# Optimization experiments

Measured on AMD Instinct MI355X. Metric: run time of the kernel, lower is better.

Reference implementation:

```python
import jax, jax.numpy as jnp
from jax import lax
import numpy as np

B, C_IN, F, T = 8, 16, 1024, 512
D = 1024          # rnn_hidden_size == rnn_input_size
L = 4             # rnn_num_layers
N_TOKENS = 512
RES_REDUCE = 2


def setup_inputs() -> dict:
    key = jax.random.key(0)
    ks = jax.random.split(key, 8)
    fused_feats = jax.random.normal(ks[0], (B, C_IN, F, T), dtype=jnp.float32)
    s_audio_length = jax.random.randint(ks[1], (B,), 1, T + 1, dtype=jnp.int64)
    # 1x1 conv: C_IN -> 1 channel
    conv_w = jax.random.normal(ks[2], (C_IN,), dtype=jnp.float32) * (1.0 / np.sqrt(C_IN))
    conv_b = jnp.zeros((1,), dtype=jnp.float32)
    # SRU per-layer params (all layers have d_in == D): W [L, D, 3D], v [L, 2D], b [L, 2D]
    sru_W = jax.random.normal(ks[3], (L, D, 3 * D), dtype=jnp.float32) * (1.0 / np.sqrt(D))
    sru_v = jax.random.normal(ks[4], (L, 2 * D), dtype=jnp.float32) * 0.1
    sru_b = jnp.zeros((L, 2 * D), dtype=jnp.float32)
    fc_w = jax.random.normal(ks[5], (D, N_TOKENS), dtype=jnp.float32) * (1.0 / np.sqrt(D))
    fc_b = jnp.zeros((N_TOKENS,), dtype=jnp.float32)
    return dict(fused_feats=fused_feats, s_audio_length=s_audio_length,
                conv_w=conv_w, conv_b=conv_b,
                sru_W=sru_W, sru_v=sru_v, sru_b=sru_b,
                fc_w=fc_w, fc_b=fc_b)


def _sru_layer(x, W, v, b):
    # x: [T, B, D]; W: [D, 3D]; v, b: [2D]
    d = W.shape[1] // 3
    U = jnp.einsum('tbi,ik->tbk', x, W).reshape(x.shape[0], x.shape[1], 3, d)
    x_tilde, f_pre, r_pre = U[..., 0, :], U[..., 1, :], U[..., 2, :]
    vf, vr = v[:d], v[d:]
    bf, br = b[:d], b[d:]

    def step(c, inp):
        xt_t, fp_t = inp
        f = jax.nn.sigmoid(fp_t + vf * c + bf)
        c_new = f * c + (1.0 - f) * xt_t
        return c_new, c_new

    c0 = jnp.zeros((x.shape[1], d), dtype=x.dtype)
    _, cs = lax.scan(step, c0, (x_tilde, f_pre))            # cs: [T, B, D]
    r = jax.nn.sigmoid(r_pre + vr * cs + br)                # reset uses c_t
    return r * cs + (1.0 - r) * x                           # highway residual


def reference(fused_feats, s_audio_length, conv_w, conv_b, sru_W, sru_v, sru_b, fc_w, fc_b):
    # 1x1 conv over channel dim + ReLU: [B, C, F, T] -> [B, F, T]
    x = jax.nn.relu(jnp.einsum('bcft,c->bft', fused_feats, conv_w) + conv_b[0])
    x = x.transpose(2, 0, 1)                                # [T, B, F]
    for l in range(L):
        x = _sru_layer(x, sru_W[l], sru_v[l], sru_b[l])
    rnn_out = x.transpose(1, 0, 2)                          # [B, T, D]
    tokens_logits = jnp.einsum('btd,dk->btk', rnn_out, fc_w) + fc_b
    return tokens_logits, s_audio_length // RES_REDUCE
```

## Files before the change

kernel.cpp:

```cpp
#include <hip/hip_runtime.h>
#include <cstddef>
#include <cstdint>

static constexpr int B_  = 8;
static constexpr int CIN = 16;
static constexpr int F_  = 1024;
static constexpr int T_  = 512;
static constexpr int D_  = 1024;
static constexpr int L_  = 4;
static constexpr int NT  = 512;
static constexpr int M_  = T_ * B_;
static constexpr int K3  = 3 * D_;
static constexpr int NP  = 4 * D_;

typedef __attribute__((ext_vector_type(8))) short short8;
typedef __attribute__((ext_vector_type(4))) float floatx4;

__device__ __forceinline__ unsigned short f2bf(float f) {
    unsigned int u = __builtin_bit_cast(unsigned int, f);
    u += 0x7FFFu + ((u >> 16) & 1u);
    return (unsigned short)(u >> 16);
}
__device__ __forceinline__ float bf2f(unsigned short s) {
    unsigned int u = ((unsigned int)s) << 16;
    return __builtin_bit_cast(float, u);
}

#define GLD16(g, l)                                                              \
    __builtin_amdgcn_global_load_lds(                                            \
        (__attribute__((address_space(1))) unsigned int*)(g),                    \
        (__attribute__((address_space(3))) unsigned int*)(l), 16, 0, 0)

__global__ __launch_bounds__(256) void conv_relu_tr(
    const float* __restrict__ feats, const float* __restrict__ wv,
    const float* __restrict__ bv, unsigned short* __restrict__ x0) {
    __shared__ float tile[32][68];
    const int b  = blockIdx.z;
    const int f0 = blockIdx.y * 32;
    const int t0 = blockIdx.x * 64;
    const float bias = bv[0];

    const int t4 = threadIdx.x & 15;
    const int fi = threadIdx.x >> 4;
    #pragma unroll
    for (int fo = 0; fo < 32; fo += 16) {
        const int f = fo + fi;
        float4 acc = {bias, bias, bias, bias};
        const float* p = feats + (((size_t)b * CIN) * F_ + (f0 + f)) * T_ + t0 + t4 * 4;
        #pragma unroll
        for (int c = 0; c < CIN; ++c) {
            const float4 vv = *(const float4*)(p + (size_t)c * F_ * T_);
            const float w = wv[c];
            acc.x += w * vv.x; acc.y += w * vv.y;
            acc.z += w * vv.z; acc.w += w * vv.w;
        }
        acc.x = fmaxf(acc.x, 0.f); acc.y = fmaxf(acc.y, 0.f);
        acc.z = fmaxf(acc.z, 0.f); acc.w = fmaxf(acc.w, 0.f);
        *(float4*)&tile[f][t4 * 4] = acc;
    }
    __syncthreads();
    const int f4 = threadIdx.x & 7;
    const int tr = threadIdx.x >> 3;
    #pragma unroll
    for (int to = 0; to < 64; to += 32) {
        const int t = to + tr;
        unsigned short pk[4];
        #pragma unroll
        for (int q = 0; q < 4; ++q) pk[q] = f2bf(tile[f4 * 4 + q][t]);
        *(uint2*)&x0[(size_t)(t0 + t) * (B_ * D_) + (size_t)b * D_ + f0 + f4 * 4] =
            *(const uint2*)pk;
    }
}

__global__ __launch_bounds__(256) void prep_weights(
    const float* __restrict__ sru_W, const float* __restrict__ fc_w,
    unsigned short* __restrict__ Wt, unsigned short* __restrict__ WtF) {
    __shared__ float tile[32][33];
    const int z  = blockIdx.z;
    const int x  = threadIdx.x & 31;
    const int y8 = threadIdx.x >> 5;
    if (z < 16) {
        const int l = z >> 2, j = z & 3;
        const int d0 = blockIdx.x * 32;
        const int k0 = blockIdx.y * 32;
        unsigned short* Wo = Wt + (size_t)l * ((size_t)NP * D_);
        if (j < 3) {
            const float* W = sru_W + (size_t)l * D_ * K3;
            #pragma unroll
            for (int yo = 0; yo < 32; yo += 8)
                tile[yo + y8][x] = W[(size_t)(k0 + yo + y8) * K3 + j * D_ + d0 + x];
            __syncthreads();
            #pragma unroll
            for (int yo = 0; yo < 32; yo += 8) {
                const int dy = yo + y8;
                Wo[(size_t)((d0 + dy) * 4 + j) * D_ + k0 + x] = f2bf(tile[x][dy]);
            }
        } else {
            #pragma unroll
            for (int yo = 0; yo < 32; yo += 8) {
                const int dy = d0 + yo + y8;
                Wo[(size_t)(dy * 4 + 3) * D_ + k0 + x] =
                    (k0 + x == dy) ? (unsigned short)0x3F80u : (unsigned short)0u;
            }
        }
    } else {
        if (blockIdx.x >= NT / 32) return;
        const int n0 = blockIdx.x * 32;
        const int k0 = blockIdx.y * 32;
        #pragma unroll
        for (int yo = 0; yo < 32; yo += 8)
            tile[yo + y8][x] = fc_w[(size_t)(k0 + yo + y8) * NT + n0 + x];
        __syncthreads();
        #pragma unroll
        for (int yo = 0; yo < 32; yo += 8)
            WtF[(size_t)(n0 + yo + y8) * D_ + k0 + x] = f2bf(tile[x][yo + y8]);
    }
}

__global__ __launch_bounds__(256) void gemm_fc(
    const unsigned short* __restrict__ A,
    const unsigned short* __restrict__ Bt,
    float* __restrict__ Cv, const float* __restrict__ bias,
    const int* __restrict__ lens, float* __restrict__ lout,
    int N, int K) {
    __shared__ unsigned short As[128 * 32];
    __shared__ unsigned short Bs[128 * 32];

    const int tid  = threadIdx.x;
    const int lane = tid & 63;
    const int wid  = tid >> 6;
    const int m0 = blockIdx.y * 128;
    const int n0 = blockIdx.x * 128;
    const int wm = (wid >> 1) * 64;
    const int wn = (wid & 1) * 64;

    if (blockIdx.x == 0 && blockIdx.y == 0 && tid < B_)
        lout[tid] = (float)(lens[tid] >> 1);

    floatx4 acc[4][4];
    #pragma unroll
    for (int mi = 0; mi < 4; ++mi)
        #pragma unroll
        for (int ni = 0; ni < 4; ++ni)
            acc[mi][ni] = (floatx4){0.f, 0.f, 0.f, 0.f};

    const char* gA = (const char*)A;
    const char* gB = (const char*)Bt;
    const size_t rowstride = (size_t)K * 2;
    const size_t rA0 = (size_t)(m0 + (tid >> 2)) * rowstride + (tid & 3) * 16;
    const size_t rB0 = (size_t)(n0 + (tid >> 2)) * rowstride + (tid & 3) * 16;
    const size_t pstep = 64 * rowstride;
    char* sA = (char*)As;
    char* sB = (char*)Bs;
    const int ldsbase = wid * 1024;

    const int rsel = lane & 15;
    const int koff = (lane >> 4) * 16;

    for (int k0 = 0; k0 < K; k0 += 32) {
        const size_t kb = (size_t)k0 * 2;
        GLD16(gA + rA0 + kb,         sA + ldsbase);
        GLD16(gA + rA0 + kb + pstep, sA + ldsbase + 4096);
        GLD16(gB + rB0 + kb,         sB + ldsbase);
        GLD16(gB + rB0 + kb + pstep, sB + ldsbase + 4096);
        __syncthreads();

        short8 af[4], bfv[4];
        #pragma unroll
        for (int mi = 0; mi < 4; ++mi)
            af[mi] = *(const short8*)(sA + ((wm + mi * 16 + rsel) * 64 + koff));
        #pragma unroll
        for (int ni = 0; ni < 4; ++ni)
            bfv[ni] = *(const short8*)(sB + ((wn + ni * 16 + rsel) * 64 + koff));
        #pragma unroll
        for (int mi = 0; mi < 4; ++mi)
            #pragma unroll
            for (int ni = 0; ni < 4; ++ni)
                acc[mi][ni] = __builtin_amdgcn_mfma_f32_16x16x32_bf16(
                    af[mi], bfv[ni], acc[mi][ni], 0, 0, 0);
        __syncthreads();
    }

    const int cl = lane & 15;
    const int qr = lane >> 4;
    #pragma unroll
    for (int mi = 0; mi < 4; ++mi) {
        #pragma unroll
        for (int ni = 0; ni < 4; ++ni) {
            const int gn = n0 + wn + ni * 16 + cl;
            #pragma unroll
            for (int i = 0; i < 4; ++i) {
                const int gm = m0 + wm + mi * 16 + qr * 4 + i;
                const int t  = gm >> 3;
                const int bb = gm & 7;
                Cv[((size_t)bb * T_ + t) * NT + gn] = acc[mi][ni][i] + bias[gn];
            }
        }
    }
}

#define KT_BODY(CB, PB, KT2, DO_STAGE)                                        \
    {                                                                         \
        if (DO_STAGE) {      \
            const size_t gk = (size_t)(KT2) * 64;                             \
            _Pragma("unroll") for (int s = 0; s < 2; ++s)                     \
                GLD16(Ab + (size_t)grow[s] * 2048 + gk + gcol[s],             \
                      (PB) + ((s * 8 + wid) << 10));                          \
        }                                                                     \
        short8 af[8], bf01[2], bf23[2];                                       \
        _Pragma("unroll") for (int mi = 0; mi < 8; ++mi)                      \
            af[mi] = *(const short8*)((CB) + aoff[mi]);                       \
        _Pragma("unroll") for (int ni = 0; ni < 2; ++ni)                      \
            bf01[ni] = *(const short8*)((CB) + boff[ni]);                     \
        __builtin_amdgcn_s_setprio(1);                                        \
        _Pragma("unroll") for (int mi = 0; mi < 8; ++mi)                      \
            _Pragma("unroll") for (int ni = 0; ni < 2; ++ni)                  \
                acc[mi][ni] = __builtin_amdgcn_mfma_f32_16x16x32_bf16(        \
                    af[mi], bf01[ni], acc[mi][ni], 0, 0, 0);                  \
        __builtin_amdgcn_s_setprio(0);                                        \
        __builtin_amdgcn_s_barrier();                                         \
        if (DO_STAGE) {      \
            const size_t gk = (size_t)(KT2) * 64;                             \
            _Pragma("unroll") for (int s = 0; s < 2; ++s)                     \
                GLD16(Bb + (size_t)grow[s] * 2048 + gk + gcol[s],             \
                      (PB) + 16384 + ((s * 8 + wid) << 10));                  \
        }                                                                     \
        _Pragma("unroll") for (int ni = 0; ni < 2; ++ni)                      \
            bf23[ni] = *(const short8*)((CB) + boff[2 + ni]);                 \
        __builtin_amdgcn_s_setprio(1);                                        \
        _Pragma("unroll") for (int mi = 0; mi < 8; ++mi)                      \
            _Pragma("unroll") for (int ni = 0; ni < 2; ++ni)                  \
                acc[mi][2 + ni] = __builtin_amdgcn_mfma_f32_16x16x32_bf16(    \
                    af[mi], bf23[ni], acc[mi][2 + ni], 0, 0, 0);              \
        __builtin_amdgcn_s_setprio(0);                                        \
    }

__global__ __launch_bounds__(512, 2) void gemm256_gate(
    const unsigned short* __restrict__ A,
    const unsigned short* __restrict__ Bt,
    unsigned short* __restrict__ C) {
    __shared__ unsigned short lds[49152];
    char* const sb = (char*)lds;

    const int tid  = threadIdx.x;
    const int lane = tid & 63;
    const int wid  = tid >> 6;
    const int wm   = wid >> 2;
    const int wn   = wid & 3;
    const int m0   = blockIdx.y * 256;
    const int n0   = blockIdx.x * 256;

    const char* Ab = (const char*)A  + (size_t)m0 * 2048;
    const char* Bb = (const char*)Bt + (size_t)n0 * 2048;

    int grow[2], gcol[2];
    #pragma unroll
    for (int s = 0; s < 2; ++s) {
        const int q  = ((s * 8 + wid) << 10) + lane * 16;
        const int qs = q ^ (((q >> 7) & 3) << 4);
        grow[s] = qs >> 6;
        gcol[s] = qs & 63;
    }
    const int rl = lane & 15;
    const int kb = (lane >> 4) * 16;
    int aoff[8], boff[4];
    #pragma unroll
    for (int mi = 0; mi < 8; ++mi) {
        const int q = (wm * 128 + mi * 16 + rl) * 64 + kb;
        aoff[mi] = q ^ (((q >> 7) & 3) << 4);
    }
    #pragma unroll
    for (int ni = 0; ni < 4; ++ni) {
        const int q = (wn * 64 + ni * 16 + rl) * 64 + kb;
        boff[ni] = 16384 + (q ^ (((q >> 7) & 3) << 4));
    }

    floatx4 acc[8][4];
    #pragma unroll
    for (int mi = 0; mi < 8; ++mi)
        #pragma unroll
        for (int ni = 0; ni < 4; ++ni)
            acc[mi][ni] = (floatx4){0.f, 0.f, 0.f, 0.f};

    char* const b0 = sb;
    char* const b1 = sb + 32768;
    char* const b2 = sb + 65536;

    #pragma unroll
    for (int t = 0; t < 2; ++t) {
        char* pb = sb + t * 32768;
        const size_t gk = (size_t)t * 64;
        #pragma unroll
        for (int s = 0; s < 2; ++s)
            GLD16(Ab + (size_t)grow[s] * 2048 + gk + gcol[s],
                  pb + ((s * 8 + wid) << 10));
        #pragma unroll
        for (int s = 0; s < 2; ++s)
            GLD16(Bb + (size_t)grow[s] * 2048 + gk + gcol[s],
                  pb + 16384 + ((s * 8 + wid) << 10));
    }
    asm volatile("s_waitcnt vmcnt(4)" ::: "memory");
    __builtin_amdgcn_s_barrier();

    for (int kt = 0; kt < 30; kt += 3) {
        KT_BODY(b0, b2, kt + 2, true);
        asm volatile("s_waitcnt vmcnt(4)" ::: "memory");
        __builtin_amdgcn_s_barrier();
        KT_BODY(b1, b0, kt + 3, true);
        asm volatile("s_waitcnt vmcnt(4)" ::: "memory");
        __builtin_amdgcn_s_barrier();
        KT_BODY(b2, b1, kt + 4, true);
        asm volatile("s_waitcnt vmcnt(4)" ::: "memory");
        __builtin_amdgcn_s_barrier();
    }
    KT_BODY(b0, b2, 0, false);
    asm volatile("s_waitcnt vmcnt(0)" ::: "memory");
    __builtin_amdgcn_s_barrier();
    KT_BODY(b1, b0, 0, false);

    const int cl = lane & 15;
    const int qr = lane >> 4;
    #pragma unroll
    for (int mi = 0; mi < 8; ++mi) {
        #pragma unroll
        for (int ni = 0; ni < 4; ++ni) {
            const int gn = n0 + wn * 64 + ni * 16 + cl;
            #pragma unroll
            for (int i = 0; i < 4; ++i) {
                const int gm = m0 + wm * 128 + mi * 16 + qr * 4 + i;
                C[(size_t)gm * NP + gn] = f2bf(acc[mi][ni][i]);
            }
        }
    }
}

__global__ __launch_bounds__(64) void sru_scan(
    const unsigned short* __restrict__ U4,
    const float* __restrict__ v, const float* __restrict__ bvec,
    unsigned short* __restrict__ h) {
    const int idx = blockIdx.x * 64 + threadIdx.x;
    const int d  = idx & (D_ - 1);

    constexpr float L2E = 1.44269504088896340736f;
    const float vf2  = -v[d] * L2E;
    const float vr2  = -v[D_ + d] * L2E;
    const float mbfL = -bvec[d] * L2E;
    const float mbrL = -bvec[D_ + d] * L2E;

    const uint2* up = (const uint2*)U4 + idx;
    unsigned short* hp = h + idx;

    constexpr int UNR  = 8;
    constexpr int PIPE = 4;
    constexpr int NB   = T_ / UNR;
    constexpr size_t ST = (size_t)B_ * D_;

    uint2 ub[PIPE][UNR];
    #pragma unroll
    for (int p = 0; p < PIPE; ++p)
        #pragma unroll
        for (int j = 0; j < UNR; ++j)
            ub[p][j] = up[(size_t)(p * UNR + j) * ST];

    float c = 0.0f;
    for (int bt = 0; bt < NB; bt += PIPE) {
        #pragma unroll
        for (int p = 0; p < PIPE; ++p) {
            const int s = bt + p;
            #pragma unroll
            for (int j = 0; j < UNR; ++j) {
                const uint2 u = ub[p][j];
                const float xt  = bf2f((unsigned short)(u.x & 0xFFFFu));
                const float fpp = bf2f((unsigned short)(u.x >> 16));
                const float rpp = bf2f((unsigned short)(u.y & 0xFFFFu));
                const float xi  = bf2f((unsigned short)(u.y >> 16));
                const float pre1 = fmaf(fpp, -L2E, mbfL);
                const float pre2 = fmaf(rpp, -L2E, mbrL);
                float e1;
                asm("v_exp_f32 %0, %1" : "=v"(e1) : "v"(fmaf(vf2, c, pre1)));
                const float f  = __builtin_amdgcn_rcpf(1.0f + e1);
                c = fmaf(f, c - xt, xt);
                float e2;
                asm("v_exp_f32 %0, %1" : "=v"(e2) : "v"(fmaf(vr2, c, pre2)));
                const float r  = __builtin_amdgcn_rcpf(1.0f + e2);
                hp[(size_t)(s * UNR + j) * ST] = f2bf(fmaf(r, c - xi, xi));
            }
            if (s + PIPE < NB) {
                #pragma unroll
                for (int j = 0; j < UNR; ++j)
                    ub[p][j] = up[(size_t)((s + PIPE) * UNR + j) * ST];
            }
        }
    }
}

extern "C" void kernel_launch(void* const* d_in, const int* in_sizes, int n_in,
                              void* d_out, int out_size, void* d_ws, size_t ws_size,
                              hipStream_t stream) {
    const float* feats  = (const float*)d_in[0];
    const int*   lens   = (const int*)d_in[1];
    const float* conv_w = (const float*)d_in[2];
    const float* conv_b = (const float*)d_in[3];
    const float* sru_W  = (const float*)d_in[4];
    const float* sru_v  = (const float*)d_in[5];
    const float* sru_b  = (const float*)d_in[6];
    const float* fc_w   = (const float*)d_in[7];
    const float* fc_b   = (const float*)d_in[8];
    float* out = (float*)d_out;

    unsigned short* x0 = (unsigned short*)d_ws;
    unsigned short* x1 = x0 + (size_t)M_ * D_;
    unsigned short* U4 = x1 + (size_t)M_ * D_;
    unsigned short* Wt = U4 + (size_t)M_ * NP;
    unsigned short* WtF = Wt + (size_t)L_ * NP * D_;

    conv_relu_tr<<<dim3(T_ / 64, F_ / 32, B_), 256, 0, stream>>>(
        feats, conv_w, conv_b, x0);

    prep_weights<<<dim3(32, 32, 17), 256, 0, stream>>>(sru_W, fc_w, Wt, WtF);

    unsigned short* cur = x0;
    unsigned short* nxt = x1;
    for (int l = 0; l < L_; ++l) {
        gemm256_gate<<<dim3(NP / 256, M_ / 256), 512, 0, stream>>>(
            cur, Wt + (size_t)l * NP * D_, U4);
        sru_scan<<<(B_ * D_) / 64, 64, 0, stream>>>(
            U4, sru_v + (size_t)l * 2 * D_, sru_b + (size_t)l * 2 * D_, nxt);
        unsigned short* tmp = cur; cur = nxt; nxt = tmp;
    }

    gemm_fc<<<dim3(NT / 128, M_ / 128), 256, 0, stream>>>(
        cur, WtF, out, fc_b, lens, out + (size_t)M_ * NT, NT, D_);
}
```

Before: 709.7 us.

## Drop identity block from gate GEMM and read residual input directly in scan

The gate GEMM used to compute a fourth output block equal to the identity copy of x, so the scan could read all four values packed together. That block is now removed, which cuts the GEMM's N from 4D to 3D with 192-wide tiles, and the scan reads the residual from the layer input buffer instead. The layout becomes interleaved x_tilde/f pairs followed by a separate r block. This saves a quarter of the GEMM FLOPs and the U writes, at the cost of three separate strided loads per step in the scan and a shallower prefetch depth there.

After: 752.6 us. 6.0% more time.

```diff
diff --git a/kernel.cpp b/kernel.cpp
--- a/kernel.cpp
+++ b/kernel.cpp
@@ -11,7 +11,7 @@
 static constexpr int NT  = 512;
 static constexpr int M_  = T_ * B_;
 static constexpr int K3  = 3 * D_;
-static constexpr int NP  = 4 * D_;
+static constexpr int N3  = 3 * D_;
 
 typedef __attribute__((ext_vector_type(8))) short short8;
 typedef __attribute__((ext_vector_type(4))) float floatx4;
@@ -79,29 +79,21 @@
     const int z  = blockIdx.z;
     const int x  = threadIdx.x & 31;
     const int y8 = threadIdx.x >> 5;
-    if (z < 16) {
-        const int l = z >> 2, j = z & 3;
+    if (z < 12) {
+        const int l = z / 3, j = z % 3;
         const int d0 = blockIdx.x * 32;
         const int k0 = blockIdx.y * 32;
-        unsigned short* Wo = Wt + (size_t)l * ((size_t)NP * D_);
-        if (j < 3) {
-            const float* W = sru_W + (size_t)l * D_ * K3;
-            #pragma unroll
-            for (int yo = 0; yo < 32; yo += 8)
-                tile[yo + y8][x] = W[(size_t)(k0 + yo + y8) * K3 + j * D_ + d0 + x];
-            __syncthreads();
-            #pragma unroll
-            for (int yo = 0; yo < 32; yo += 8) {
-                const int dy = yo + y8;
-                Wo[(size_t)((d0 + dy) * 4 + j) * D_ + k0 + x] = f2bf(tile[x][dy]);
-            }
-        } else {
-            #pragma unroll
-            for (int yo = 0; yo < 32; yo += 8) {
-                const int dy = d0 + yo + y8;
-                Wo[(size_t)(dy * 4 + 3) * D_ + k0 + x] =
-                    (k0 + x == dy) ? (unsigned short)0x3F80u : (unsigned short)0u;
-            }
+        unsigned short* Wo = Wt + (size_t)l * ((size_t)N3 * D_);
+        const float* W = sru_W + (size_t)l * D_ * K3;
+        #pragma unroll
+        for (int yo = 0; yo < 32; yo += 8)
+            tile[yo + y8][x] = W[(size_t)(k0 + yo + y8) * K3 + j * D_ + d0 + x];
+        __syncthreads();
+        #pragma unroll
+        for (int yo = 0; yo < 32; yo += 8) {
+            const int dy = d0 + yo + y8;
+            const int n = (j < 2) ? (dy * 2 + j) : (2048 + dy);
+            Wo[(size_t)n * D_ + k0 + x] = f2bf(tile[x][yo + y8]);
         }
     } else {
         if (blockIdx.x >= NT / 32) return;
@@ -204,10 +196,10 @@
         if (DO_STAGE) {      \
             const size_t gk = (size_t)(KT2) * 64;                             \
             _Pragma("unroll") for (int s = 0; s < 2; ++s)                     \
-                GLD16(Ab + (size_t)grow[s] * 2048 + gk + gcol[s],             \
+                GLD16(Ab + (size_t)arow[s] * 2048 + gk + acol[s],             \
                       (PB) + ((s * 8 + wid) << 10));                          \
         }                                                                     \
-        short8 af[8], bf01[2], bf23[2];                                       \
+        short8 af[8], bf01[2], bf2;                                           \
         _Pragma("unroll") for (int mi = 0; mi < 8; ++mi)                      \
             af[mi] = *(const short8*)((CB) + aoff[mi]);                       \
         _Pragma("unroll") for (int ni = 0; ni < 2; ++ni)                      \
@@ -222,20 +214,18 @@
         if (DO_STAGE) {      \
             const size_t gk = (size_t)(KT2) * 64;                             \
             _Pragma("unroll") for (int s = 0; s < 2; ++s)                     \
-                GLD16(Bb + (size_t)grow[s] * 2048 + gk + gcol[s],             \
+                GLD16(Bb + (size_t)brow[s] * 2048 + gk + bcol[s],             \
                       (PB) + 16384 + ((s * 8 + wid) << 10));                  \
         }                                                                     \
-        _Pragma("unroll") for (int ni = 0; ni < 2; ++ni)                      \
-            bf23[ni] = *(const short8*)((CB) + boff[2 + ni]);                 \
+        bf2 = *(const short8*)((CB) + boff[2]);                               \
         __builtin_amdgcn_s_setprio(1);                                        \
         _Pragma("unroll") for (int mi = 0; mi < 8; ++mi)                      \
-            _Pragma("unroll") for (int ni = 0; ni < 2; ++ni)                  \
-                acc[mi][2 + ni] = __builtin_amdgcn_mfma_f32_16x16x32_bf16(    \
-                    af[mi], bf23[ni], acc[mi][2 + ni], 0, 0, 0);              \
+            acc[mi][2] = __builtin_amdgcn_mfma_f32_16x16x32_bf16(             \
+                af[mi], bf2, acc[mi][2], 0, 0, 0);                            \
         __builtin_amdgcn_s_setprio(0);                                        \
     }
 
-__global__ __launch_bounds__(512, 2) void gemm256_gate(
+__global__ __launch_bounds__(512, 2) void gemm192_gate(
     const unsigned short* __restrict__ A,
     const unsigned short* __restrict__ Bt,
     unsigned short* __restrict__ C) {
@@ -248,38 +238,40 @@
     const int wm   = wid >> 2;
     const int wn   = wid & 3;
     const int m0   = blockIdx.y * 256;
-    const int n0   = blockIdx.x * 256;
+    const int n0   = blockIdx.x * 192;
 
     const char* Ab = (const char*)A  + (size_t)m0 * 2048;
     const char* Bb = (const char*)Bt + (size_t)n0 * 2048;
 
-    int grow[2], gcol[2];
+    int arow[2], acol[2], brow[2], bcol[2];
     #pragma unroll
     for (int s = 0; s < 2; ++s) {
         const int q  = ((s * 8 + wid) << 10) + lane * 16;
         const int qs = q ^ (((q >> 7) & 3) << 4);
-        grow[s] = qs >> 6;
-        gcol[s] = qs & 63;
+        arow[s] = qs >> 6;
+        acol[s] = qs & 63;
+        brow[s] = (q < 12288) ? (qs >> 6) : 0;
+        bcol[s] = qs & 63;
     }
     const int rl = lane & 15;
     const int kb = (lane >> 4) * 16;
-    int aoff[8], boff[4];
+    int aoff[8], boff[3];
     #pragma unroll
     for (int mi = 0; mi < 8; ++mi) {
         const int q = (wm * 128 + mi * 16 + rl) * 64 + kb;
         aoff[mi] = q ^ (((q >> 7) & 3) << 4);
     }
     #pragma unroll
-    for (int ni = 0; ni < 4; ++ni) {
-        const int q = (wn * 64 + ni * 16 + rl) * 64 + kb;
+    for (int ni = 0; ni < 3; ++ni) {
+        const int q = (wn * 48 + ni * 16 + rl) * 64 + kb;
         boff[ni] = 16384 + (q ^ (((q >> 7) & 3) << 4));
     }
 
-    floatx4 acc[8][4];
+    floatx4 acc[8][3];
     #pragma unroll
     for (int mi = 0; mi < 8; ++mi)
         #pragma unroll
-        for (int ni = 0; ni < 4; ++ni)
+        for (int ni = 0; ni < 3; ++ni)
             acc[mi][ni] = (floatx4){0.f, 0.f, 0.f, 0.f};
 
     char* const b0 = sb;
@@ -292,11 +284,11 @@
         const size_t gk = (size_t)t * 64;
         #pragma unroll
         for (int s = 0; s < 2; ++s)
-            GLD16(Ab + (size_t)grow[s] * 2048 + gk + gcol[s],
+            GLD16(Ab + (size_t)arow[s] * 2048 + gk + acol[s],
                   pb + ((s * 8 + wid) << 10));
         #pragma unroll
         for (int s = 0; s < 2; ++s)
-            GLD16(Bb + (size_t)grow[s] * 2048 + gk + gcol[s],
+            GLD16(Bb + (size_t)brow[s] * 2048 + gk + bcol[s],
                   pb + 16384 + ((s * 8 + wid) << 10));
     }
     asm volatile("s_waitcnt vmcnt(4)" ::: "memory");
@@ -323,23 +315,25 @@
     #pragma unroll
     for (int mi = 0; mi < 8; ++mi) {
         #pragma unroll
-        for (int ni = 0; ni < 4; ++ni) {
-            const int gn = n0 + wn * 64 + ni * 16 + cl;
+        for (int ni = 0; ni < 3; ++ni) {
+            const int gn = n0 + wn * 48 + ni * 16 + cl;
             #pragma unroll
             for (int i = 0; i < 4; ++i) {
                 const int gm = m0 + wm * 128 + mi * 16 + qr * 4 + i;
-                C[(size_t)gm * NP + gn] = f2bf(acc[mi][ni][i]);
+                C[(size_t)gm * N3 + gn] = f2bf(acc[mi][ni][i]);
             }
         }
     }
 }
 
 __global__ __launch_bounds__(64) void sru_scan(
-    const unsigned short* __restrict__ U4,
+    const unsigned short* __restrict__ U3,
+    const unsigned short* __restrict__ xin,
     const float* __restrict__ v, const float* __restrict__ bvec,
     unsigned short* __restrict__ h) {
     const int idx = blockIdx.x * 64 + threadIdx.x;
-    const int d  = idx & (D_ - 1);
+    const int d = idx & (D_ - 1);
+    const int b = idx >> 10;
 
     constexpr float L2E = 1.44269504088896340736f;
     const float vf2  = -v[d] * L2E;
@@ -347,20 +341,30 @@
     const float mbfL = -bvec[d] * L2E;
     const float mbrL = -bvec[D_ + d] * L2E;
 
-    const uint2* up = (const uint2*)U4 + idx;
-    unsigned short* hp = h + idx;
+    const unsigned int*   uf = (const unsigned int*)U3 + (size_t)b * (N3 / 2) + d;
+    const unsigned short* ur = U3 + (size_t)b * N3 + 2048 + d;
+    const unsigned short* ux = xin + (size_t)b * D_ + d;
+    unsigned short*       hp = h + (size_t)b * D_ + d;
 
     constexpr int UNR  = 8;
-    constexpr int PIPE = 4;
+    constexpr int PIPE = 2;
     constexpr int NB   = T_ / UNR;
-    constexpr size_t ST = (size_t)B_ * D_;
-
-    uint2 ub[PIPE][UNR];
+    constexpr size_t SU = (size_t)B_ * (N3 / 2);
+    constexpr size_t SR = (size_t)B_ * N3;
+    constexpr size_t SX = (size_t)B_ * D_;
+
+    unsigned int   ub[PIPE][UNR];
+    unsigned short rb[PIPE][UNR];
+    unsigned short xb[PIPE][UNR];
     #pragma unroll
     for (int p = 0; p < PIPE; ++p)
         #pragma unroll
-        for (int j = 0; j < UNR; ++j)
-            ub[p][j] = up[(size_t)(p * UNR + j) * ST];
+        for (int j = 0; j < UNR; ++j) {
+            const size_t t = (size_t)(p * UNR + j);
+            ub[p][j] = uf[t * SU];
+            rb[p][j] = ur[t * SR];
+            xb[p][j] = ux[t * SX];
+        }
 
     float c = 0.0f;
     for (int bt = 0; bt < NB; bt += PIPE) {
@@ -369,11 +373,11 @@
             const int s = bt + p;
             #pragma unroll
             for (int j = 0; j < UNR; ++j) {
-                const uint2 u = ub[p][j];
-                const float xt  = bf2f((unsigned short)(u.x & 0xFFFFu));
-                const float fpp = bf2f((unsigned short)(u.x >> 16));
-                const float rpp = bf2f((unsigned short)(u.y & 0xFFFFu));
-                const float xi  = bf2f((unsigned short)(u.y >> 16));
+                const unsigned int u = ub[p][j];
+                const float xt  = bf2f((unsigned short)(u & 0xFFFFu));
+                const float fpp = bf2f((unsigned short)(u >> 16));
+                const float rpp = bf2f(rb[p][j]);
+                const float xi  = bf2f(xb[p][j]);
                 const float pre1 = fmaf(fpp, -L2E, mbfL);
                 const float pre2 = fmaf(rpp, -L2E, mbrL);
                 float e1;
@@ -383,12 +387,16 @@
                 float e2;
                 asm("v_exp_f32 %0, %1" : "=v"(e2) : "v"(fmaf(vr2, c, pre2)));
                 const float r  = __builtin_amdgcn_rcpf(1.0f + e2);
-                hp[(size_t)(s * UNR + j) * ST] = f2bf(fmaf(r, c - xi, xi));
+                hp[(size_t)(s * UNR + j) * SX] = f2bf(fmaf(r, c - xi, xi));
             }
             if (s + PIPE < NB) {
                 #pragma unroll
-                for (int j = 0; j < UNR; ++j)
-                    ub[p][j] = up[(size_t)((s + PIPE) * UNR + j) * ST];
+                for (int j = 0; j < UNR; ++j) {
+                    const size_t t = (size_t)((s + PIPE) * UNR + j);
+                    ub[p][j] = uf[t * SU];
+                    rb[p][j] = ur[t * SR];
+                    xb[p][j] = ux[t * SX];
+                }
             }
         }
     }
@@ -410,22 +418,22 @@
 
     unsigned short* x0 = (unsigned short*)d_ws;
     unsigned short* x1 = x0 + (size_t)M_ * D_;
-    unsigned short* U4 = x1 + (size_t)M_ * D_;
-    unsigned short* Wt = U4 + (size_t)M_ * NP;
-    unsigned short* WtF = Wt + (size_t)L_ * NP * D_;
+    unsigned short* U3 = x1 + (size_t)M_ * D_;
+    unsigned short* Wt = U3 + (size_t)M_ * N3;
+    unsigned short* WtF = Wt + (size_t)L_ * N3 * D_;
 
     conv_relu_tr<<<dim3(T_ / 64, F_ / 32, B_), 256, 0, stream>>>(
         feats, conv_w, conv_b, x0);
 
-    prep_weights<<<dim3(32, 32, 17), 256, 0, stream>>>(sru_W, fc_w, Wt, WtF);
+    prep_weights<<<dim3(32, 32, 13), 256, 0, stream>>>(sru_W, fc_w, Wt, WtF);
 
     unsigned short* cur = x0;
     unsigned short* nxt = x1;
     for (int l = 0; l < L_; ++l) {
-        gemm256_gate<<<dim3(NP / 256, M_ / 256), 512, 0, stream>>>(
-            cur, Wt + (size_t)l * NP * D_, U4);
+        gemm192_gate<<<dim3(N3 / 192, M_ / 256), 512, 0, stream>>>(
+            cur, Wt + (size_t)l * N3 * D_, U3);
         sru_scan<<<(B_ * D_) / 64, 64, 0, stream>>>(
-            U4, sru_v + (size_t)l * 2 * D_, sru_b + (size_t)l * 2 * D_, nxt);
+            U3, cur, sru_v + (size_t)l * 2 * D_, sru_b + (size_t)l * 2 * D_, nxt);
         unsigned short* tmp = cur; cur = nxt; nxt = tmp;
     }
 
```

## Fuse SRU gate GEMM with scan via per-column completion counters

Applied to the files above, without the earlier changes.

Merges the conv/ReLU/transpose kernel and the weight-prep kernel into one launch. Also fuses each layer's gate GEMM and recurrent scan into a single kernel. Every GEMM block bumps an atomic counter for its output column. The last of the 16 row blocks to finish a column then runs the scan for that column's 64 hidden units across all 8 batches. This removes kernel launch gaps and lets scans start while other columns are still in the GEMM, at the cost of putting the serial scan on only 16 workgroups and relying on cross-block memory fences for correctness.

Result: slower. 890.1 us (+25.4%).

```diff
diff --git a/kernel.cpp b/kernel.cpp
--- a/kernel.cpp
+++ b/kernel.cpp
@@ -31,56 +31,61 @@
         (__attribute__((address_space(1))) unsigned int*)(g),                    \
         (__attribute__((address_space(3))) unsigned int*)(l), 16, 0, 0)
 
-__global__ __launch_bounds__(256) void conv_relu_tr(
+__global__ __launch_bounds__(256) void conv_prep(
     const float* __restrict__ feats, const float* __restrict__ wv,
-    const float* __restrict__ bv, unsigned short* __restrict__ x0) {
-    __shared__ float tile[32][68];
-    const int b  = blockIdx.z;
-    const int f0 = blockIdx.y * 32;
-    const int t0 = blockIdx.x * 64;
-    const float bias = bv[0];
-
-    const int t4 = threadIdx.x & 15;
-    const int fi = threadIdx.x >> 4;
-    #pragma unroll
-    for (int fo = 0; fo < 32; fo += 16) {
-        const int f = fo + fi;
-        float4 acc = {bias, bias, bias, bias};
-        const float* p = feats + (((size_t)b * CIN) * F_ + (f0 + f)) * T_ + t0 + t4 * 4;
-        #pragma unroll
-        for (int c = 0; c < CIN; ++c) {
-            const float4 vv = *(const float4*)(p + (size_t)c * F_ * T_);
-            const float w = wv[c];
-            acc.x += w * vv.x; acc.y += w * vv.y;
-            acc.z += w * vv.z; acc.w += w * vv.w;
-        }
-        acc.x = fmaxf(acc.x, 0.f); acc.y = fmaxf(acc.y, 0.f);
-        acc.z = fmaxf(acc.z, 0.f); acc.w = fmaxf(acc.w, 0.f);
-        *(float4*)&tile[f][t4 * 4] = acc;
-    }
-    __syncthreads();
-    const int f4 = threadIdx.x & 7;
-    const int tr = threadIdx.x >> 3;
-    #pragma unroll
-    for (int to = 0; to < 64; to += 32) {
-        const int t = to + tr;
-        unsigned short pk[4];
-        #pragma unroll
-        for (int q = 0; q < 4; ++q) pk[q] = f2bf(tile[f4 * 4 + q][t]);
-        *(uint2*)&x0[(size_t)(t0 + t) * (B_ * D_) + (size_t)b * D_ + f0 + f4 * 4] =
-            *(const uint2*)pk;
-    }
-}
-
-__global__ __launch_bounds__(256) void prep_weights(
+    const float* __restrict__ bv, unsigned short* __restrict__ x0,
     const float* __restrict__ sru_W, const float* __restrict__ fc_w,
-    unsigned short* __restrict__ Wt, unsigned short* __restrict__ WtF) {
-    __shared__ float tile[32][33];
-    const int z  = blockIdx.z;
+    unsigned short* __restrict__ Wt, unsigned short* __restrict__ WtF,
+    int* __restrict__ ready) {
+    __shared__ float tileA[32][68];
+    __shared__ float tileB[32][33];
+    const int z = blockIdx.z;
+
+    if (z < 8) {
+        if (blockIdx.x >= 8) return;
+        const int b  = z;
+        const int f0 = blockIdx.y * 32;
+        const int t0 = blockIdx.x * 64;
+        const float bias = bv[0];
+
+        const int t4 = threadIdx.x & 15;
+        const int fi = threadIdx.x >> 4;
+        #pragma unroll
+        for (int fo = 0; fo < 32; fo += 16) {
+            const int f = fo + fi;
+            float4 acc = {bias, bias, bias, bias};
+            const float* p =
+                feats + (((size_t)b * CIN) * F_ + (f0 + f)) * T_ + t0 + t4 * 4;
+            #pragma unroll
+            for (int c = 0; c < CIN; ++c) {
+                const float4 vv = *(const float4*)(p + (size_t)c * F_ * T_);
+                const float w = wv[c];
+                acc.x += w * vv.x; acc.y += w * vv.y;
+                acc.z += w * vv.z; acc.w += w * vv.w;
+            }
+            acc.x = fmaxf(acc.x, 0.f); acc.y = fmaxf(acc.y, 0.f);
+            acc.z = fmaxf(acc.z, 0.f); acc.w = fmaxf(acc.w, 0.f);
+            *(float4*)&tileA[f][t4 * 4] = acc;
+        }
+        __syncthreads();
+        const int f4 = threadIdx.x & 7;
+        const int tr = threadIdx.x >> 3;
+        #pragma unroll
+        for (int to = 0; to < 64; to += 32) {
+            const int t = to + tr;
+            unsigned short pk[4];
+            #pragma unroll
+            for (int q = 0; q < 4; ++q) pk[q] = f2bf(tileA[f4 * 4 + q][t]);
+            *(uint2*)&x0[(size_t)(t0 + t) * (B_ * D_) + (size_t)b * D_ +
+                         f0 + f4 * 4] = *(const uint2*)pk;
+        }
+        return;
+    }
+
     const int x  = threadIdx.x & 31;
     const int y8 = threadIdx.x >> 5;
-    if (z < 16) {
-        const int l = z >> 2, j = z & 3;
+    if (z < 24) {
+        const int l = (z - 8) >> 2, j = (z - 8) & 3;
         const int d0 = blockIdx.x * 32;
         const int k0 = blockIdx.y * 32;
         unsigned short* Wo = Wt + (size_t)l * ((size_t)NP * D_);
@@ -88,12 +93,12 @@
             const float* W = sru_W + (size_t)l * D_ * K3;
             #pragma unroll
             for (int yo = 0; yo < 32; yo += 8)
-                tile[yo + y8][x] = W[(size_t)(k0 + yo + y8) * K3 + j * D_ + d0 + x];
+                tileB[yo + y8][x] = W[(size_t)(k0 + yo + y8) * K3 + j * D_ + d0 + x];
             __syncthreads();
             #pragma unroll
             for (int yo = 0; yo < 32; yo += 8) {
                 const int dy = yo + y8;
-                Wo[(size_t)((d0 + dy) * 4 + j) * D_ + k0 + x] = f2bf(tile[x][dy]);
+                Wo[(size_t)((d0 + dy) * 4 + j) * D_ + k0 + x] = f2bf(tileB[x][dy]);
             }
         } else {
             #pragma unroll
@@ -104,25 +109,25 @@
             }
         }
     } else {
+        if (blockIdx.x == 0 && blockIdx.y == 0 && threadIdx.x < 64)
+            ready[threadIdx.x] = 0;
         if (blockIdx.x >= NT / 32) return;
         const int n0 = blockIdx.x * 32;
         const int k0 = blockIdx.y * 32;
         #pragma unroll
         for (int yo = 0; yo < 32; yo += 8)
-            tile[yo + y8][x] = fc_w[(size_t)(k0 + yo + y8) * NT + n0 + x];
+            tileB[yo + y8][x] = fc_w[(size_t)(k0 + yo + y8) * NT + n0 + x];
         __syncthreads();
         #pragma unroll
         for (int yo = 0; yo < 32; yo += 8)
-            WtF[(size_t)(n0 + yo + y8) * D_ + k0 + x] = f2bf(tile[x][yo + y8]);
+            WtF[(size_t)(n0 + yo + y8) * D_ + k0 + x] = f2bf(tileB[x][yo + y8]);
     }
 }
 
 __global__ __launch_bounds__(256) void gemm_fc(
-    const unsigned short* __restrict__ A,
-    const unsigned short* __restrict__ Bt,
+    const unsigned short* __restrict__ A, const unsigned short* __restrict__ Bt,
     float* __restrict__ Cv, const float* __restrict__ bias,
-    const int* __restrict__ lens, float* __restrict__ lout,
-    int N, int K) {
+    const int* __restrict__ lens, float* __restrict__ lout, int N, int K) {
     __shared__ unsigned short As[128 * 32];
     __shared__ unsigned short Bs[128 * 32];
 
@@ -235,20 +240,17 @@
         __builtin_amdgcn_s_setprio(0);                                        \
     }
 
-__global__ __launch_bounds__(512, 2) void gemm256_gate(
-    const unsigned short* __restrict__ A,
-    const unsigned short* __restrict__ Bt,
-    unsigned short* __restrict__ C) {
-    __shared__ unsigned short lds[49152];
-    char* const sb = (char*)lds;
-
+__device__ __forceinline__ void gemm_gate_body(
+    int bid, const unsigned short* __restrict__ A,
+    const unsigned short* __restrict__ Bt, unsigned short* __restrict__ C,
+    char* sb) {
     const int tid  = threadIdx.x;
     const int lane = tid & 63;
     const int wid  = tid >> 6;
     const int wm   = wid >> 2;
     const int wn   = wid & 3;
-    const int m0   = blockIdx.y * 256;
-    const int n0   = blockIdx.x * 256;
+    const int m0   = (bid >> 4) * 256;
+    const int n0   = (bid & 15) * 256;
 
     const char* Ab = (const char*)A  + (size_t)m0 * 2048;
     const char* Bb = (const char*)Bt + (size_t)n0 * 2048;
@@ -334,12 +336,10 @@
     }
 }
 
-__global__ __launch_bounds__(64) void sru_scan(
-    const unsigned short* __restrict__ U4,
-    const float* __restrict__ v, const float* __restrict__ bvec,
-    unsigned short* __restrict__ h) {
-    const int idx = blockIdx.x * 64 + threadIdx.x;
-    const int d  = idx & (D_ - 1);
+__device__ __forceinline__ void scan_body(
+    const unsigned short* __restrict__ U4, const float* __restrict__ v,
+    const float* __restrict__ bvec, unsigned short* __restrict__ h, int idx) {
+    const int d = idx & (D_ - 1);
 
     constexpr float L2E = 1.44269504088896340736f;
     const float vf2  = -v[d] * L2E;
@@ -394,6 +394,34 @@
     }
 }
 
+__global__ __launch_bounds__(512, 2) void gemm_gate_scan(
+    const unsigned short* __restrict__ A, const unsigned short* __restrict__ Bt,
+    unsigned short* U4, const float* __restrict__ v,
+    const float* __restrict__ bvec, unsigned short* __restrict__ H,
+    int* __restrict__ ready) {
+    __shared__ unsigned short lds[49152];
+    __shared__ int last;
+    const int bid = blockIdx.y * 16 + blockIdx.x;
+
+    gemm_gate_body(bid, A, Bt, U4, (char*)lds);
+
+    __syncthreads();
+    if (threadIdx.x == 0) {
+        __threadfence();
+        const int old = __hip_atomic_fetch_add(
+            &ready[blockIdx.x], 1, __ATOMIC_ACQ_REL, __HIP_MEMORY_SCOPE_AGENT);
+        last = (old == 15) ? 1 : 0;
+        if (old == 15) __threadfence();
+    }
+    __syncthreads();
+
+    if (last) {
+        const int d = blockIdx.x * 64 + ((int)threadIdx.x & 63);
+        const int b = (int)threadIdx.x >> 6;
+        scan_body(U4, v, bvec, H, b * D_ + d);
+    }
+}
+
 extern "C" void kernel_launch(void* const* d_in, const int* in_sizes, int n_in,
                               void* d_out, int out_size, void* d_ws, size_t ws_size,
                               hipStream_t stream) {
@@ -413,19 +441,18 @@
     unsigned short* U4 = x1 + (size_t)M_ * D_;
     unsigned short* Wt = U4 + (size_t)M_ * NP;
     unsigned short* WtF = Wt + (size_t)L_ * NP * D_;
-
-    conv_relu_tr<<<dim3(T_ / 64, F_ / 32, B_), 256, 0, stream>>>(
-        feats, conv_w, conv_b, x0);
-
-    prep_weights<<<dim3(32, 32, 17), 256, 0, stream>>>(sru_W, fc_w, Wt, WtF);
+    int* ready = (int*)(WtF + (size_t)NT * D_);
+
+    conv_prep<<<dim3(32, 32, 25), 256, 0, stream>>>(
+        feats, conv_w, conv_b, x0, sru_W, fc_w, Wt, WtF, ready);
 
     unsigned short* cur = x0;
     unsigned short* nxt = x1;
     for (int l = 0; l < L_; ++l) {
-        gemm256_gate<<<dim3(NP / 256, M_ / 256), 512, 0, stream>>>(
-            cur, Wt + (size_t)l * NP * D_, U4);
-        sru_scan<<<(B_ * D_) / 64, 64, 0, stream>>>(
-            U4, sru_v + (size_t)l * 2 * D_, sru_b + (size_t)l * 2 * D_, nxt);
+        gemm_gate_scan<<<dim3(16, 16), 512, 0, stream>>>(
+            cur, Wt + (size_t)l * NP * D_, U4,
+            sru_v + (size_t)l * 2 * D_, sru_b + (size_t)l * 2 * D_,
+            nxt, ready + l * 16);
         unsigned short* tmp = cur; cur = nxt; nxt = tmp;
     }
 
```
